# Performance work log

Measured on AMD Instinct MI355X. Metric: run time of the kernel, lower is better.

The kernel has to match this reference:

```python
import jax, jax.numpy as jnp
import numpy as np


def setup_inputs() -> dict:
    key = jax.random.key(0)
    k1, k2, k3, k4, k5 = jax.random.split(key, 5)
    B, S, E, U = 32, 2048, 1024, 1024
    last_hidden_state = jax.random.normal(k1, (B, S, E), dtype=jnp.float32)
    attention_mask = jax.random.randint(k2, (B, S), 0, 2, dtype=jnp.int32)
    # ensure at least one valid token per row to avoid all -inf softmax
    attention_mask = attention_mask.at[:, 0].set(1)
    W = jax.random.normal(k3, (U, E), dtype=jnp.float32) * (E ** -0.5)
    Umat = jax.random.normal(k4, (U, E), dtype=jnp.float32) * (E ** -0.5)
    v = jax.random.normal(k5, (1, U), dtype=jnp.float32) * (U ** -0.5)
    return {"last_hidden_state": last_hidden_state, "attention_mask": attention_mask,
            "W": W, "U": Umat, "v": v}


def reference(last_hidden_state, attention_mask, W, U, v):
    # last_hidden_state: [B,S,E]; W,U: [units,E]; v: [1,units]
    Q = jnp.einsum('bse,ue->bsu', last_hidden_state, W)
    K = jnp.einsum('bse,ue->bsu', last_hidden_state, U)
    H = jnp.tanh(Q + K)                                   # [B,S,units]
    E = jnp.einsum('bsu,ou->bso', H, v)                   # [B,S,1]
    neg_inf = jnp.array(-jnp.inf, dtype=E.dtype)
    E = jnp.where(attention_mask[:, :, None] == 0, neg_inf, E)
    alpha = jax.nn.softmax(E, axis=1)                     # softmax over seq dim
    return jnp.sum(alpha * last_hidden_state, axis=1)     # [B,E]
```

## Files before the change

### kernel.cpp

```cpp
#include <hip/hip_runtime.h>
#include <hip/hip_bf16.h>


typedef short bf16x8 __attribute__((ext_vector_type(8)));
typedef float f32x4  __attribute__((ext_vector_type(4)));
typedef unsigned short u16x8 __attribute__((ext_vector_type(8)));

static __device__ __forceinline__ unsigned short f2bf(float f) {
    unsigned int x = __float_as_uint(f);
    unsigned int r = x + 0x7FFFu + ((x >> 16) & 1u);
    return (unsigned short)(r >> 16);
}

static __device__ __forceinline__ float fast_tanh(float x) {
    float e = __builtin_amdgcn_exp2f(x * 2.885390082f);
    float r = __builtin_amdgcn_rcpf(e + 1.0f);
    return __builtin_fmaf(-2.0f, r, 1.0f);
}

__global__ __launch_bounds__(256)
void prep_index(const float* __restrict__ W, const float* __restrict__ U,
                const int* __restrict__ mask,
                unsigned short* __restrict__ Bt, unsigned short* __restrict__ wsumrm,
                float* __restrict__ score, float* __restrict__ out,
                unsigned short* __restrict__ ridx, int* __restrict__ cnt) {
    __shared__ int sc[256];
    int blk = blockIdx.x, t = threadIdx.x;
    if (blk < 1024) {
        int g = blk * 256 + t;
        int i4 = g * 4;
        float4 w = *(const float4*)&W[i4];
        float4 u = *(const float4*)&U[i4];
        ushort4 h;
        h.x = f2bf(w.x + u.x); h.y = f2bf(w.y + u.y);
        h.z = f2bf(w.z + u.z); h.w = f2bf(w.w + u.w);
        *(ushort4*)&wsumrm[i4] = h;
        int n  = i4 >> 10;
        int k0 = i4 & 1023;
        *(ushort4*)&Bt[(size_t)(k0 >> 3) * 8192 + n * 8 + (k0 & 7)] = h;
        if (g < 65536) score[g] = 0.0f;
        if (g < 32768) out[g] = 0.0f;
    } else {
        int b = blk - 1024;
        const int* mrow = mask + b * 2048;
        int m[8], c = 0;
#pragma unroll
        for (int j = 0; j < 8; ++j) { m[j] = mrow[t * 8 + j]; c += (m[j] != 0); }
        sc[t] = c;
        __syncthreads();
        for (int off = 1; off < 256; off <<= 1) {
            int v = (t >= off) ? sc[t - off] : 0;
            __syncthreads();
            sc[t] += v;
            __syncthreads();
        }
        int base = sc[t] - c;
        unsigned short* rb = ridx + b * 2048;
#pragma unroll
        for (int j = 0; j < 8; ++j)
            if (m[j]) rb[base++] = (unsigned short)(t * 8 + j);
        if (t == 255) cnt[b] = sc[255];
    }
}

__global__ __launch_bounds__(256)
void gather_convert(const float* __restrict__ lhs, const unsigned short* __restrict__ ridx,
                    const int* __restrict__ cnt, unsigned short* __restrict__ Ab) {
    int b = blockIdx.y;
    int c = cnt[b];
    int cpad = (c + 127) & ~127;
    int r = blockIdx.x * 4 + (threadIdx.x >> 6);
    int lt = threadIdx.x & 63;
    if (r >= cpad) return;
    unsigned short* dst = Ab + ((size_t)b * 2048 + r) * 1024 + lt * 16;
    if (r < c) {
        int s = ridx[b * 2048 + r];
        const float* src = lhs + ((size_t)b * 2048 + s) * 1024 + lt * 16;
        float4 a0 = *(const float4*)(src + 0);
        float4 a1 = *(const float4*)(src + 4);
        float4 a2 = *(const float4*)(src + 8);
        float4 a3 = *(const float4*)(src + 12);
        u16x8 h0, h1;
        h0[0] = f2bf(a0.x); h0[1] = f2bf(a0.y); h0[2] = f2bf(a0.z); h0[3] = f2bf(a0.w);
        h0[4] = f2bf(a1.x); h0[5] = f2bf(a1.y); h0[6] = f2bf(a1.z); h0[7] = f2bf(a1.w);
        h1[0] = f2bf(a2.x); h1[1] = f2bf(a2.y); h1[2] = f2bf(a2.z); h1[3] = f2bf(a2.w);
        h1[4] = f2bf(a3.x); h1[5] = f2bf(a3.y); h1[6] = f2bf(a3.z); h1[7] = f2bf(a3.w);
        *(u16x8*)(dst + 0) = h0;
        *(u16x8*)(dst + 8) = h1;
    } else {
        u16x8 z = (u16x8){0,0,0,0,0,0,0,0};
        *(u16x8*)(dst + 0) = z;
        *(u16x8*)(dst + 8) = z;
    }
}

__global__ __launch_bounds__(256)
void score_gemm_v3(const unsigned short* __restrict__ Ab,
                   const unsigned short* __restrict__ Bt,
                   const float* __restrict__ v, const int* __restrict__ cnt,
                   float* __restrict__ score) {
    const int K = 1024;
    __shared__ __align__(16) unsigned short As[128 * 64];

    const int bid    = (int)blockIdx.x;
    const int group  = bid >> 6;
    const int mt     = (group << 3) + (bid & 7);
    const int nI     = (bid >> 3) & 7;
    const int b      = mt >> 4;
    const int lm0    = (mt & 15) << 7;
    const int c      = cnt[b];
    if (lm0 >= ((c + 127) & ~127)) return;
    const int m0     = (b << 11) + lm0;
    const int n0     = nI << 7;

    const int t    = threadIdx.x;
    const int lane = t & 63;
    const int wave = t >> 6;
    const int wm   = (wave & 1) * 64;
    const int wn   = (wave >> 1) * 64;
    const int ml   = lane & 15;
    const int q    = lane >> 4;
    const int xorv = ml & 7;

    f32x4 acc[4][4];
#pragma unroll
    for (int i = 0; i < 4; ++i)
#pragma unroll
        for (int j = 0; j < 4; ++j)
            acc[i][j] = (f32x4){0.f, 0.f, 0.f, 0.f};

    const unsigned short* gA[4];
    unsigned short* lA[4];
#pragma unroll
    for (int p = 0; p < 4; ++p) {
        int l   = p * 256 + wave * 64 + lane;
        int row = l >> 3;
        int kc  = (l & 7) ^ (row & 7);
        gA[p] = Ab + (size_t)(m0 + row) * K + kc * 8;
        lA[p] = &As[(p * 4 + wave) * 512];
    }

    const unsigned short* bp[4];
#pragma unroll
    for (int j = 0; j < 4; ++j)
        bp[j] = Bt + (size_t)q * 8192 + (n0 + wn + j * 16 + ml) * 8;

    for (int kk = 0; kk < K; kk += 64) {
#pragma unroll
        for (int p = 0; p < 4; ++p) {
            __builtin_amdgcn_global_load_lds((const __attribute__((address_space(1))) unsigned int*)gA[p],
                                             (__attribute__((address_space(3))) unsigned int*)lA[p], 16, 0, 0);
            gA[p] += 64;
        }
        __syncthreads();

#pragma unroll
        for (int s = 0; s < 2; ++s) {
            bf16x8 bf[4];
#pragma unroll
            for (int j = 0; j < 4; ++j)
                bf[j] = *(const bf16x8*)(bp[j] + (size_t)s * 32768);
            const int koff = ((s * 4 + q) ^ xorv) * 8;
            bf16x8 af[4];
#pragma unroll
            for (int i = 0; i < 4; ++i)
                af[i] = *(const bf16x8*)&As[(wm + i * 16 + ml) * 64 + koff];
#pragma unroll
            for (int i = 0; i < 4; ++i)
#pragma unroll
                for (int j = 0; j < 4; ++j)
                    acc[i][j] = __builtin_amdgcn_mfma_f32_16x16x32_bf16(af[i], bf[j], acc[i][j], 0, 0, 0);
        }
#pragma unroll
        for (int j = 0; j < 4; ++j)
            bp[j] += 65536;
        __syncthreads();
    }

    float vw[4];
#pragma unroll
    for (int j = 0; j < 4; ++j)
        vw[j] = v[n0 + wn + j * 16 + ml];

#pragma unroll
    for (int i = 0; i < 4; ++i) {
#pragma unroll
        for (int r = 0; r < 4; ++r) {
            float val = 0.f;
#pragma unroll
            for (int j = 0; j < 4; ++j)
                val += fast_tanh(acc[i][j][r]) * vw[j];
#pragma unroll
            for (int off = 8; off > 0; off >>= 1)
                val += __shfl_xor(val, off, 64);
            if (ml == 0)
                atomicAdd(&score[m0 + wm + i * 16 + q * 4 + r], val);
        }
    }
}

__global__ __launch_bounds__(256)
void softmax_wsum(const float* __restrict__ score, const int* __restrict__ cnt,
                  const unsigned short* __restrict__ Ab, float* __restrict__ out) {
    __shared__ float red[8];
    __shared__ float al[2048];
    int b   = blockIdx.x >> 4;
    int seg = blockIdx.x & 15;
    int t   = threadIdx.x;
    int c   = cnt[b];

    float sc[8];
    float mx = -1e30f;
#pragma unroll
    for (int i = 0; i < 8; ++i) {
        int k = i * 256 + t;
        sc[i] = (k < c) ? score[b * 2048 + k] : -1e30f;
        mx = fmaxf(mx, sc[i]);
    }
#pragma unroll
    for (int off = 32; off > 0; off >>= 1)
        mx = fmaxf(mx, __shfl_xor(mx, off, 64));
    if ((t & 63) == 0) red[t >> 6] = mx;
    __syncthreads();
    mx = fmaxf(fmaxf(red[0], red[1]), fmaxf(red[2], red[3]));
    float e[8], sum = 0.f;
#pragma unroll
    for (int i = 0; i < 8; ++i) {
        int k = i * 256 + t;
        e[i] = (k < c) ? __expf(sc[i] - mx) : 0.f;
        sum += e[i];
    }
#pragma unroll
    for (int off = 32; off > 0; off >>= 1)
        sum += __shfl_xor(sum, off, 64);
    if ((t & 63) == 0) red[4 + (t >> 6)] = sum;
    __syncthreads();
    float inv = 1.0f / (red[4] + red[5] + red[6] + red[7]);
#pragma unroll
    for (int i = 0; i < 8; ++i)
        al[i * 256 + t] = e[i] * inv;
    __syncthreads();

    int per = (c + 15) >> 4;
    int s0  = seg * per;
    int s1  = min(s0 + per, c);
    const unsigned short* base = Ab + (size_t)b * 2048 * 1024 + t * 4;
    float a0 = 0.f, a1 = 0.f, a2 = 0.f, a3 = 0.f;
    for (int s = s0; s < s1; ++s) {
        float a = al[s];
        ushort4 h = *(const ushort4*)(base + (size_t)s * 1024);
        a0 = __builtin_fmaf(a, __uint_as_float((unsigned)h.x << 16), a0);
        a1 = __builtin_fmaf(a, __uint_as_float((unsigned)h.y << 16), a1);
        a2 = __builtin_fmaf(a, __uint_as_float((unsigned)h.z << 16), a2);
        a3 = __builtin_fmaf(a, __uint_as_float((unsigned)h.w << 16), a3);
    }
    float* o = out + b * 1024 + t * 4;
    atomicAdd(o + 0, a0);
    atomicAdd(o + 1, a1);
    atomicAdd(o + 2, a2);
    atomicAdd(o + 3, a3);
}

#define LDSS 40
__global__ __launch_bounds__(256)
void score_gemm_f32stage(const float* __restrict__ A, const unsigned short* __restrict__ Bw,
                         const float* __restrict__ v, float* __restrict__ score) {
    const int K = 1024;
    __shared__ __align__(16) unsigned short As[128][LDSS];
    __shared__ __align__(16) unsigned short Bs[128][LDSS];
    const int n0 = (int)blockIdx.x * 128;
    const int m0 = (int)blockIdx.y * 128;
    const int t = threadIdx.x, lane = t & 63, wave = t >> 6;
    const int wm = (wave & 1) * 64, wn = (wave >> 1) * 64;
    const int ml = lane & 15, q = lane >> 4;
    f32x4 acc[4][4];
#pragma unroll
    for (int i = 0; i < 4; ++i)
#pragma unroll
        for (int j = 0; j < 4; ++j) acc[i][j] = (f32x4){0.f,0.f,0.f,0.f};
    const int sr = t >> 3, sc = (t & 7) * 4;
    for (int kk = 0; kk < K; kk += 32) {
#pragma unroll
        for (int p = 0; p < 4; ++p) {
            int r = sr + p * 32;
            float4 va = *(const float4*)&A[(size_t)(m0 + r) * K + kk + sc];
            ushort4 h; h.x = f2bf(va.x); h.y = f2bf(va.y); h.z = f2bf(va.z); h.w = f2bf(va.w);
            *(ushort4*)&As[r][sc] = h;
            ushort4 vb = *(const ushort4*)&Bw[(size_t)(n0 + r) * K + kk + sc];
            *(ushort4*)&Bs[r][sc] = vb;
        }
        __syncthreads();
        bf16x8 af[4], bf[4];
#pragma unroll
        for (int i = 0; i < 4; ++i) af[i] = *(const bf16x8*)&As[wm + i * 16 + ml][q * 8];
#pragma unroll
        for (int j = 0; j < 4; ++j) bf[j] = *(const bf16x8*)&Bs[wn + j * 16 + ml][q * 8];
#pragma unroll
        for (int i = 0; i < 4; ++i)
#pragma unroll
            for (int j = 0; j < 4; ++j)
                acc[i][j] = __builtin_amdgcn_mfma_f32_16x16x32_bf16(af[i], bf[j], acc[i][j], 0, 0, 0);
        __syncthreads();
    }
    float vw[4];
#pragma unroll
    for (int j = 0; j < 4; ++j) vw[j] = v[n0 + wn + j * 16 + ml];
#pragma unroll
    for (int i = 0; i < 4; ++i)
#pragma unroll
        for (int r = 0; r < 4; ++r) {
            float val = 0.f;
#pragma unroll
            for (int j = 0; j < 4; ++j) val += fast_tanh(acc[i][j][r]) * vw[j];
#pragma unroll
            for (int off = 8; off > 0; off >>= 1) val += __shfl_xor(val, off, 64);
            if (ml == 0) atomicAdd(&score[m0 + wm + i * 16 + q * 4 + r], val);
        }
}

__global__ __launch_bounds__(256)
void softmax_kernel(const float* __restrict__ score, const int* __restrict__ mask,
                    float* __restrict__ alpha) {
    const int S = 2048;
    int b = blockIdx.x, t = threadIdx.x;
    __shared__ float red[8];
    float sc[8]; int vd[8];
    float mx = -1e30f;
#pragma unroll
    for (int i = 0; i < 8; ++i) {
        int s = i * 256 + t;
        vd[i] = mask[b * S + s];
        sc[i] = score[b * S + s];
        if (vd[i]) mx = fmaxf(mx, sc[i]);
    }
#pragma unroll
    for (int off = 32; off > 0; off >>= 1)
        mx = fmaxf(mx, __shfl_xor(mx, off, 64));
    if ((t & 63) == 0) red[t >> 6] = mx;
    __syncthreads();
    mx = fmaxf(fmaxf(red[0], red[1]), fmaxf(red[2], red[3]));
    float e[8]; float sum = 0.f;
#pragma unroll
    for (int i = 0; i < 8; ++i) {
        e[i] = vd[i] ? __expf(sc[i] - mx) : 0.f;
        sum += e[i];
    }
#pragma unroll
    for (int off = 32; off > 0; off >>= 1)
        sum += __shfl_xor(sum, off, 64);
    if ((t & 63) == 0) red[4 + (t >> 6)] = sum;
    __syncthreads();
    float inv = 1.0f / (red[4] + red[5] + red[6] + red[7]);
#pragma unroll
    for (int i = 0; i < 8; ++i)
        alpha[b * S + i * 256 + t] = e[i] * inv;
}

__global__ __launch_bounds__(256)
void wsum_kernel(const float* __restrict__ lhs, const float* __restrict__ alpha,
                 float* __restrict__ out) {
    const int S = 2048, E = 1024;
    int b = blockIdx.x >> 6;
    int seg = blockIdx.x & 63;
    int t = threadIdx.x;
    int s0 = seg * 32;
    const float* base = lhs + ((size_t)b * S + s0) * E + t * 4;
    const float* ap = alpha + b * S + s0;
    float4 acc = {0.f, 0.f, 0.f, 0.f};
#pragma unroll 4
    for (int s = 0; s < 32; ++s) {
        float a = ap[s];
        if (a != 0.f) {
            float4 x = *(const float4*)(base + (size_t)s * E);
            acc.x += a * x.x; acc.y += a * x.y; acc.z += a * x.z; acc.w += a * x.w;
        }
    }
    float* o = out + b * E + t * 4;
    atomicAdd(o + 0, acc.x);
    atomicAdd(o + 1, acc.y);
    atomicAdd(o + 2, acc.z);
    atomicAdd(o + 3, acc.w);
}

extern "C" void kernel_launch(void* const* d_in, const int* in_sizes, int n_in,
                              void* d_out, int out_size, void* d_ws, size_t ws_size,
                              hipStream_t stream) {
    const float* lhs  = (const float*)d_in[0];
    const int*   mask = (const int*)d_in[1];
    const float* W    = (const float*)d_in[2];
    const float* Um   = (const float*)d_in[3];
    const float* v    = (const float*)d_in[4];
    float* out = (float*)d_out;

    char* ws = (char*)d_ws;
    unsigned short* Bt     = (unsigned short*)ws;
    unsigned short* wsumrm = (unsigned short*)(ws + 2048u * 1024u);
    float* score           = (float*)(ws + 4096u * 1024u);
    float* alphac          = (float*)(ws + 4352u * 1024u);
    unsigned short* ridx   = (unsigned short*)(ws + 4608u * 1024u);
    int* cnt               = (int*)(ws + 4736u * 1024u);
    unsigned short* Ab     = (unsigned short*)(ws + 5120u * 1024u);
    const size_t need = 5120ull * 1024ull + 131072ull * 1024ull;

    prep_index<<<1056, 256, 0, stream>>>(W, Um, mask, Bt, wsumrm, score, out, ridx, cnt);
    if (ws_size >= need) {
        dim3 gg(512, 32);
        gather_convert<<<gg, 256, 0, stream>>>(lhs, ridx, cnt, Ab);
        score_gemm_v3<<<4096, 256, 0, stream>>>(Ab, Bt, v, cnt, score);
        softmax_wsum<<<512, 256, 0, stream>>>(score, cnt, Ab, out);
    } else {
        dim3 g1(8, 512);
        score_gemm_f32stage<<<g1, 256, 0, stream>>>(lhs, wsumrm, v, score);
        softmax_kernel<<<32, 256, 0, stream>>>(score, mask, alphac);
        wsum_kernel<<<2048, 256, 0, stream>>>(lhs, alphac, out);
    }
}
```

Before: 495.9 us.

## Replace score GEMM with 256x256-tile double-buffered LDS pipeline for both operands

The score GEMM now uses 512-thread blocks with 256x256 output tiles. Both A and B are staged into 128KB of LDS through global_load_lds with XOR swizzling, and the K loop is double-buffered with explicit vmcnt/lgkmcnt waits, barriers and setprio around the MFMA phases. The B operand is now read from the row-major wsum buffer instead of a pre-transposed copy, which removes the Bt write from the prep kernel. Padding of valid rows grows to multiples of 256, so up to 255 extra zero rows per batch may be computed, and the large LDS footprint limits how many blocks fit per CU.

```diff
diff --git a/kernel.cpp b/kernel.cpp
--- a/kernel.cpp
+++ b/kernel.cpp
@@ -21,7 +21,7 @@
 __global__ __launch_bounds__(256)
 void prep_index(const float* __restrict__ W, const float* __restrict__ U,
                 const int* __restrict__ mask,
-                unsigned short* __restrict__ Bt, unsigned short* __restrict__ wsumrm,
+                unsigned short* __restrict__ wsumrm,
                 float* __restrict__ score, float* __restrict__ out,
                 unsigned short* __restrict__ ridx, int* __restrict__ cnt) {
     __shared__ int sc[256];
@@ -35,9 +35,6 @@
         h.x = f2bf(w.x + u.x); h.y = f2bf(w.y + u.y);
         h.z = f2bf(w.z + u.z); h.w = f2bf(w.w + u.w);
         *(ushort4*)&wsumrm[i4] = h;
-        int n  = i4 >> 10;
-        int k0 = i4 & 1023;
-        *(ushort4*)&Bt[(size_t)(k0 >> 3) * 8192 + n * 8 + (k0 & 7)] = h;
         if (g < 65536) score[g] = 0.0f;
         if (g < 32768) out[g] = 0.0f;
     } else {
@@ -68,7 +65,7 @@
                     const int* __restrict__ cnt, unsigned short* __restrict__ Ab) {
     int b = blockIdx.y;
     int c = cnt[b];
-    int cpad = (c + 127) & ~127;
+    int cpad = (c + 255) & ~255;
     int r = blockIdx.x * 4 + (threadIdx.x >> 6);
     int lt = threadIdx.x & 63;
     if (r >= cpad) return;
@@ -94,109 +91,161 @@
     }
 }
 
-__global__ __launch_bounds__(256)
-void score_gemm_v3(const unsigned short* __restrict__ Ab,
-                   const unsigned short* __restrict__ Bt,
+#define GLD(SRC, LOFF) __builtin_amdgcn_global_load_lds( \
+    (const __attribute__((address_space(1))) unsigned int*)(SRC), \
+    (__attribute__((address_space(3))) unsigned int*)&L[LOFF], 16, 0, 0)
+
+#define STAGE_A(BUF, MQ, KT) do { \
+    GLD(gA[MQ][0] + (KT) * 64, ((BUF) << 14) + ((MQ) << 13) + (wv << 9)); \
+    GLD(gA[MQ][1] + (KT) * 64, ((BUF) << 14) + ((MQ) << 13) + 4096 + (wv << 9)); \
+} while (0)
+
+#define STAGE_B(BUF, NQ, KT) do { \
+    GLD(gB[NQ][0] + (KT) * 64, 32768 + ((BUF) << 14) + ((NQ) << 13) + (wv << 9)); \
+    GLD(gB[NQ][1] + (KT) * 64, 32768 + ((BUF) << 14) + ((NQ) << 13) + 4096 + (wv << 9)); \
+} while (0)
+
+#define VM4 asm volatile("s_waitcnt vmcnt(4)" ::: "memory");
+#define VM0 asm volatile("s_waitcnt vmcnt(0)" ::: "memory");
+#define VMNONE
+#define NOSTAGE
+
+#define PHASE(MQ, NQ, STAGES, VMW) do { \
+    bf16x8 af[4][2]; bf16x8 bfr[2][2]; \
+    const int ab_ = (buf << 14) + ((MQ) << 13) + arow_; \
+    const int bb_ = 32768 + (buf << 14) + ((NQ) << 13) + brow_; \
+    _Pragma("unroll") for (int i_ = 0; i_ < 4; ++i_) { \
+        af[i_][0] = *(const bf16x8*)&L[ab_ + i_ * 1024 + koff0]; \
+        af[i_][1] = *(const bf16x8*)&L[ab_ + i_ * 1024 + koff1]; \
+    } \
+    _Pragma("unroll") for (int j_ = 0; j_ < 2; ++j_) { \
+        bfr[j_][0] = *(const bf16x8*)&L[bb_ + j_ * 1024 + koff0]; \
+        bfr[j_][1] = *(const bf16x8*)&L[bb_ + j_ * 1024 + koff1]; \
+    } \
+    __builtin_amdgcn_sched_barrier(0); \
+    STAGES \
+    VMW \
+    asm volatile("s_waitcnt lgkmcnt(8)" ::: "memory"); \
+    __builtin_amdgcn_s_barrier(); \
+    asm volatile("s_waitcnt lgkmcnt(0)" ::: "memory"); \
+    __builtin_amdgcn_sched_barrier(0); \
+    __builtin_amdgcn_s_setprio(1); \
+    _Pragma("unroll") for (int i_ = 0; i_ < 4; ++i_) \
+    _Pragma("unroll") for (int j_ = 0; j_ < 2; ++j_) { \
+        acc[MQ][NQ][i_][j_] = __builtin_amdgcn_mfma_f32_16x16x32_bf16(af[i_][0], bfr[j_][0], acc[MQ][NQ][i_][j_], 0, 0, 0); \
+        acc[MQ][NQ][i_][j_] = __builtin_amdgcn_mfma_f32_16x16x32_bf16(af[i_][1], bfr[j_][1], acc[MQ][NQ][i_][j_], 0, 0, 0); \
+    } \
+    __builtin_amdgcn_s_setprio(0); \
+    __builtin_amdgcn_s_barrier(); \
+    __builtin_amdgcn_sched_barrier(0); \
+} while (0)
+
+__global__ __launch_bounds__(512, 2)
+void score_gemm_v4(const unsigned short* __restrict__ Ab,
+                   const unsigned short* __restrict__ Bw,
                    const float* __restrict__ v, const int* __restrict__ cnt,
                    float* __restrict__ score) {
-    const int K = 1024;
-    __shared__ __align__(16) unsigned short As[128 * 64];
-
-    const int bid    = (int)blockIdx.x;
-    const int group  = bid >> 6;
-    const int mt     = (group << 3) + (bid & 7);
-    const int nI     = (bid >> 3) & 7;
-    const int b      = mt >> 4;
-    const int lm0    = (mt & 15) << 7;
-    const int c      = cnt[b];
-    if (lm0 >= ((c + 127) & ~127)) return;
-    const int m0     = (b << 11) + lm0;
-    const int n0     = nI << 7;
-
-    const int t    = threadIdx.x;
+    __shared__ __align__(16) unsigned short L[65536];
+
+    const int bid = (int)blockIdx.x;
+    const int li  = (bid & 7) * 128 + (bid >> 3);
+    const int mt  = li >> 2;
+    const int nI  = li & 3;
+    const int b   = mt >> 3;
+    const int lm0 = (mt & 7) << 8;
+    const int c   = cnt[b];
+    if (lm0 >= ((c + 255) & ~255)) return;
+    const int m0  = (b << 11) + lm0;
+    const int n0  = nI << 8;
+
+    const int t    = (int)threadIdx.x;
     const int lane = t & 63;
-    const int wave = t >> 6;
-    const int wm   = (wave & 1) * 64;
-    const int wn   = (wave >> 1) * 64;
+    const int wv   = t >> 6;
+    const int wm   = wv >> 2;
+    const int wn   = wv & 3;
     const int ml   = lane & 15;
     const int q    = lane >> 4;
-    const int xorv = ml & 7;
-
-    f32x4 acc[4][4];
-#pragma unroll
-    for (int i = 0; i < 4; ++i)
-#pragma unroll
-        for (int j = 0; j < 4; ++j)
-            acc[i][j] = (f32x4){0.f, 0.f, 0.f, 0.f};
-
-    const unsigned short* gA[4];
-    unsigned short* lA[4];
-#pragma unroll
-    for (int p = 0; p < 4; ++p) {
-        int l   = p * 256 + wave * 64 + lane;
-        int row = l >> 3;
-        int kc  = (l & 7) ^ (row & 7);
-        gA[p] = Ab + (size_t)(m0 + row) * K + kc * 8;
-        lA[p] = &As[(p * 4 + wave) * 512];
-    }
-
-    const unsigned short* bp[4];
-#pragma unroll
-    for (int j = 0; j < 4; ++j)
-        bp[j] = Bt + (size_t)q * 8192 + (n0 + wn + j * 16 + ml) * 8;
-
-    for (int kk = 0; kk < K; kk += 64) {
-#pragma unroll
-        for (int p = 0; p < 4; ++p) {
-            __builtin_amdgcn_global_load_lds((const __attribute__((address_space(1))) unsigned int*)gA[p],
-                                             (__attribute__((address_space(3))) unsigned int*)lA[p], 16, 0, 0);
-            gA[p] += 64;
+
+    const int lr0 = t >> 3;
+    const int ks  = (t & 7) ^ (lr0 & 7);
+    const unsigned short* gA[2][2];
+    const unsigned short* gB[2][2];
+#pragma unroll
+    for (int h = 0; h < 2; ++h)
+#pragma unroll
+        for (int j = 0; j < 2; ++j) {
+            gA[h][j] = Ab + (size_t)(m0 + h * 128 + lr0 + j * 64) * 1024 + ks * 8;
+            gB[h][j] = Bw + (size_t)(n0 + h * 128 + lr0 + j * 64) * 1024 + ks * 8;
         }
-        __syncthreads();
-
-#pragma unroll
-        for (int s = 0; s < 2; ++s) {
-            bf16x8 bf[4];
-#pragma unroll
-            for (int j = 0; j < 4; ++j)
-                bf[j] = *(const bf16x8*)(bp[j] + (size_t)s * 32768);
-            const int koff = ((s * 4 + q) ^ xorv) * 8;
-            bf16x8 af[4];
-#pragma unroll
-            for (int i = 0; i < 4; ++i)
-                af[i] = *(const bf16x8*)&As[(wm + i * 16 + ml) * 64 + koff];
-#pragma unroll
-            for (int i = 0; i < 4; ++i)
-#pragma unroll
-                for (int j = 0; j < 4; ++j)
-                    acc[i][j] = __builtin_amdgcn_mfma_f32_16x16x32_bf16(af[i], bf[j], acc[i][j], 0, 0, 0);
-        }
-#pragma unroll
-        for (int j = 0; j < 4; ++j)
-            bp[j] += 65536;
-        __syncthreads();
-    }
-
-    float vw[4];
-#pragma unroll
-    for (int j = 0; j < 4; ++j)
-        vw[j] = v[n0 + wn + j * 16 + ml];
-
-#pragma unroll
-    for (int i = 0; i < 4; ++i) {
-#pragma unroll
-        for (int r = 0; r < 4; ++r) {
-            float val = 0.f;
-#pragma unroll
-            for (int j = 0; j < 4; ++j)
-                val += fast_tanh(acc[i][j][r]) * vw[j];
-#pragma unroll
-            for (int off = 8; off > 0; off >>= 1)
-                val += __shfl_xor(val, off, 64);
-            if (ml == 0)
-                atomicAdd(&score[m0 + wm + i * 16 + q * 4 + r], val);
-        }
-    }
+
+    const int xorv  = (ml & 7) << 4;
+    const int koff0 = (((q << 4)) ^ xorv) >> 1;
+    const int koff1 = ((64 + (q << 4)) ^ xorv) >> 1;
+    const int arow_ = ((wm << 6) + ml) * 64;
+    const int brow_ = ((wn << 5) + ml) * 64;
+
+    f32x4 acc[2][2][4][2];
+#pragma unroll
+    for (int x0 = 0; x0 < 2; ++x0)
+#pragma unroll
+        for (int x1 = 0; x1 < 2; ++x1)
+#pragma unroll
+            for (int x2 = 0; x2 < 4; ++x2)
+#pragma unroll
+                for (int x3 = 0; x3 < 2; ++x3)
+                    acc[x0][x1][x2][x3] = (f32x4){0.f, 0.f, 0.f, 0.f};
+
+    STAGE_A(0, 0, 0); STAGE_B(0, 0, 0); STAGE_A(0, 1, 0); STAGE_B(0, 1, 0);
+    STAGE_A(1, 0, 1); STAGE_B(1, 0, 1);
+    VM4
+    __builtin_amdgcn_s_barrier();
+
+    for (int kt = 0; kt < 14; ++kt) {
+        const int buf  = kt & 1;
+        const int bufn = buf ^ 1;
+        PHASE(0, 0, STAGE_A(bufn, 1, kt + 1);, VMNONE);
+        PHASE(0, 1, STAGE_B(bufn, 1, kt + 1);, VMNONE);
+        PHASE(1, 0, STAGE_A(buf, 0, kt + 2);,  VMNONE);
+        PHASE(1, 1, STAGE_B(buf, 0, kt + 2);,  VM4);
+    }
+    {
+        const int buf = 0;
+        PHASE(0, 0, STAGE_A(1, 1, 15);, VMNONE);
+        PHASE(0, 1, STAGE_B(1, 1, 15);, VMNONE);
+        PHASE(1, 0, NOSTAGE;, VMNONE);
+        PHASE(1, 1, NOSTAGE;, VM0);
+    }
+    {
+        const int buf = 1;
+        PHASE(0, 0, NOSTAGE;, VMNONE);
+        PHASE(0, 1, NOSTAGE;, VMNONE);
+        PHASE(1, 0, NOSTAGE;, VMNONE);
+        PHASE(1, 1, NOSTAGE;, VMNONE);
+    }
+
+    float vw[2][2];
+#pragma unroll
+    for (int nq = 0; nq < 2; ++nq)
+#pragma unroll
+        for (int j = 0; j < 2; ++j)
+            vw[nq][j] = v[n0 + nq * 128 + (wn << 5) + j * 16 + ml];
+
+#pragma unroll
+    for (int mq = 0; mq < 2; ++mq)
+#pragma unroll
+        for (int i = 0; i < 4; ++i)
+#pragma unroll
+            for (int r = 0; r < 4; ++r) {
+                float val = fast_tanh(acc[mq][0][i][0][r]) * vw[0][0]
+                          + fast_tanh(acc[mq][0][i][1][r]) * vw[0][1]
+                          + fast_tanh(acc[mq][1][i][0][r]) * vw[1][0]
+                          + fast_tanh(acc[mq][1][i][1][r]) * vw[1][1];
+#pragma unroll
+                for (int off = 8; off > 0; off >>= 1)
+                    val += __shfl_xor(val, off, 64);
+                if (ml == 0)
+                    atomicAdd(&score[m0 + mq * 128 + (wm << 6) + i * 16 + (q << 2) + r], val);
+            }
 }
 
 __global__ __launch_bounds__(256)
@@ -278,16 +327,16 @@
     for (int i = 0; i < 4; ++i)
 #pragma unroll
         for (int j = 0; j < 4; ++j) acc[i][j] = (f32x4){0.f,0.f,0.f,0.f};
-    const int sr = t >> 3, sc = (t & 7) * 4;
+    const int sr = t >> 3, scc = (t & 7) * 4;
     for (int kk = 0; kk < K; kk += 32) {
 #pragma unroll
         for (int p = 0; p < 4; ++p) {
             int r = sr + p * 32;
-            float4 va = *(const float4*)&A[(size_t)(m0 + r) * K + kk + sc];
+            float4 va = *(const float4*)&A[(size_t)(m0 + r) * K + kk + scc];
             ushort4 h; h.x = f2bf(va.x); h.y = f2bf(va.y); h.z = f2bf(va.z); h.w = f2bf(va.w);
-            *(ushort4*)&As[r][sc] = h;
-            ushort4 vb = *(const ushort4*)&Bw[(size_t)(n0 + r) * K + kk + sc];
-            *(ushort4*)&Bs[r][sc] = vb;
+            *(ushort4*)&As[r][scc] = h;
+            ushort4 vb = *(const ushort4*)&Bw[(size_t)(n0 + r) * K + kk + scc];
+            *(ushort4*)&Bs[r][scc] = vb;
         }
         __syncthreads();
         bf16x8 af[4], bf[4];
@@ -393,7 +442,6 @@
     float* out = (float*)d_out;
 
     char* ws = (char*)d_ws;
-    unsigned short* Bt     = (unsigned short*)ws;
     unsigned short* wsumrm = (unsigned short*)(ws + 2048u * 1024u);
     float* score           = (float*)(ws + 4096u * 1024u);
     float* alphac          = (float*)(ws + 4352u * 1024u);
@@ -402,11 +450,11 @@
     unsigned short* Ab     = (unsigned short*)(ws + 5120u * 1024u);
     const size_t need = 5120ull * 1024ull + 131072ull * 1024ull;
 
-    prep_index<<<1056, 256, 0, stream>>>(W, Um, mask, Bt, wsumrm, score, out, ridx, cnt);
+    prep_index<<<1056, 256, 0, stream>>>(W, Um, mask, wsumrm, score, out, ridx, cnt);
     if (ws_size >= need) {
         dim3 gg(512, 32);
         gather_convert<<<gg, 256, 0, stream>>>(lhs, ridx, cnt, Ab);
-        score_gemm_v3<<<4096, 256, 0, stream>>>(Ab, Bt, v, cnt, score);
+        score_gemm_v4<<<1024, 512, 0, stream>>>(Ab, wsumrm, v, cnt, score);
         softmax_wsum<<<512, 256, 0, stream>>>(score, cnt, Ab, out);
     } else {
         dim3 g1(8, 512);
```

Measured after the change: 496.9 us. About the same (+0.2%).
